# Kernel optimization log

Measured on AMD Instinct MI355X. Metric: run time of the kernel, lower is better.

Reference implementation:

```python
import jax, jax.numpy as jnp
import numpy as np

B, L, LH, D, H = 32, 512, 2048, 1024, 4
DK = D // H  # dot-attn head dim
NEG = -1e9


def _ln(x, g, b, eps=1e-5):
    m = x.mean(-1, keepdims=True)
    v = ((x - m) ** 2).mean(-1, keepdims=True)
    return (x - m) / jnp.sqrt(v + eps) * g + b


def setup_inputs() -> dict:
    key = jax.random.key(0)
    ks = jax.random.split(key, 16)
    s = 0.05
    inp = {
        "seq_emb": jax.random.normal(ks[0], (B, L, D), jnp.float32),
        "seq_mask": jnp.ones((B, L), jnp.float32),
        "his_seq_emb": jax.random.normal(ks[1], (B, LH, D), jnp.float32),
        "his_seq_mask": jnp.ones((B, LH), jnp.float32),
        # dot-product MHA (bias=True)
        "sa_wq": jax.random.normal(ks[2], (D, D), jnp.float32) * s,
        "sa_bq": jnp.zeros((D,), jnp.float32),
        "sa_wk": jax.random.normal(ks[3], (D, D), jnp.float32) * s,
        "sa_bk": jnp.zeros((D,), jnp.float32),
        "sa_wv": jax.random.normal(ks[4], (D, D), jnp.float32) * s,
        "sa_bv": jnp.zeros((D,), jnp.float32),
        "sa_wo": jax.random.normal(ks[5], (D, D), jnp.float32) * s,
        "sa_bo": jnp.zeros((D,), jnp.float32),
        # short LayerNorm
        "sn_g": jnp.ones((D,), jnp.float32),
        "sn_b": jnp.zeros((D,), jnp.float32),
        # additive MHA (h=1, bias=False)
        "aa_wq": jax.random.normal(ks[6], (D, D), jnp.float32) * s,
        "aa_wk": jax.random.normal(ks[7], (D, D), jnp.float32) * s,
        "aa_wv": jax.random.normal(ks[8], (D, D), jnp.float32) * s,
        "aa_wo": jax.random.normal(ks[9], (D, D), jnp.float32) * s,
        "aa_wa": jax.random.normal(ks[10], (D,), jnp.float32) * s,
        # long LayerNorm
        "ln_g": jnp.ones((D,), jnp.float32),
        "ln_b": jnp.zeros((D,), jnp.float32),
    }
    return inp


def reference(seq_emb, seq_mask, his_seq_emb, his_seq_mask,
              sa_wq, sa_bq, sa_wk, sa_bk, sa_wv, sa_bv, sa_wo, sa_bo,
              sn_g, sn_b, aa_wq, aa_wk, aa_wv, aa_wo, aa_wa, ln_g, ln_b):
    # ---- dot-product self attention over seq_emb (dropout = eval/no-op) ----
    def split_heads(x):  # (B,L,D) -> (B,H,L,DK)
        return x.reshape(B, -1, H, DK).transpose(0, 2, 1, 3)

    q = split_heads(seq_emb @ sa_wq + sa_bq)
    k = split_heads(seq_emb @ sa_wk + sa_bk)
    v = split_heads(seq_emb @ sa_wv + sa_bv)
    scores = jnp.einsum('bhqd,bhkd->bhqk', q, k) / jnp.sqrt(jnp.float32(DK))
    scores = jnp.where(seq_mask[:, None, None, :] == 0, NEG, scores)
    p_attn = jax.nn.softmax(scores, axis=-1)  # (B,H,L,L)
    ctx = jnp.einsum('bhqk,bhkd->bhqd', p_attn, v)
    ctx = ctx.transpose(0, 2, 1, 3).reshape(B, L, D)
    sa_out = ctx @ sa_wo + sa_bo

    poi_attn = _ln(sa_out, sn_g, sn_b) * seq_mask[:, :, None]
    poi_hidden = poi_attn.mean(axis=1, keepdims=True)  # (B,1,D)

    # ---- additive (Bahdanau) attention, h=1, Lq=1 ----
    aq = poi_hidden @ aa_wq        # (B,1,D)
    ak = his_seq_emb @ aa_wk       # (B,LH,D)
    av = his_seq_emb @ aa_wv       # (B,LH,D)
    feats = jnp.tanh(aq[:, :, None, :] + ak[:, None, :, :])  # (B,1,LH,D)
    a_scores = jnp.einsum('bqkd,d->bqk', feats, aa_wa)        # (B,1,LH)
    a_scores = jnp.where(his_seq_mask[:, None, :] == 0, NEG, a_scores)
    a_w = jax.nn.softmax(a_scores, axis=-1)
    a_ctx = jnp.einsum('bqk,bkd->bqd', a_w, av)               # (B,1,D)
    aa_out = a_ctx @ aa_wo

    his_poi_hidden = poi_hidden + _ln(aa_out, ln_g, ln_b)     # (B,1,D)

    attn_weight = p_attn[:, 0, :, :]                          # (B,L,L)
    seq_hidden = jnp.concatenate([poi_hidden, his_poi_hidden], axis=-1)[:, 0, :]  # (B,2D)
    return seq_hidden, attn_weight
```

## Files before the change

kernel.cpp:

```cpp
#include <hip/hip_runtime.h>

#define NEGV (-1000000000.0f)

typedef __attribute__((ext_vector_type(8))) short sh8;
typedef __attribute__((ext_vector_type(4))) short sh4;
typedef __attribute__((ext_vector_type(8))) __bf16 bf16x8;
typedef __attribute__((ext_vector_type(4))) float f32x4;

__device__ __forceinline__ float b2f(unsigned short u) {
  unsigned v = ((unsigned)u) << 16;
  return __builtin_bit_cast(float, v);
}
__device__ __forceinline__ unsigned short f2b(float f) {
  unsigned x = __builtin_bit_cast(unsigned, f);
  unsigned r = (x + 0x7fffu + ((x >> 16) & 1u)) >> 16;
  return (unsigned short)r;
}
__device__ __forceinline__ void g2l16(const void* g, void* l) {
  __builtin_amdgcn_global_load_lds((const __attribute__((address_space(1))) unsigned int*)g,
                                   (__attribute__((address_space(3))) unsigned int*)l, 16, 0, 0);
}
__device__ __forceinline__ f32x4 mfma16(bf16x8 a, bf16x8 b, f32x4 c) {
  return __builtin_amdgcn_mfma_f32_16x16x32_bf16(a, b, c, 0, 0, 0);
}
__device__ __forceinline__ float fast_tanh(float x) {
  x = fminf(fmaxf(x, -15.f), 15.f);
  float e = __expf(2.f * x);
  return (e - 1.f) / (e + 1.f);
}

__global__ void cvt_all(const float* __restrict__ sa, unsigned short* __restrict__ da, int n4a,
                        const float* __restrict__ sb, unsigned short* __restrict__ db, int n4b)
{
  int stride = gridDim.x * blockDim.x;
  int i0 = blockIdx.x * blockDim.x + threadIdx.x;
  for (int i = i0; i < n4a; i += stride) {
    float4 v = ((const float4*)sa)[i];
    sh4 o;
    o[0] = (short)f2b(v.x); o[1] = (short)f2b(v.y);
    o[2] = (short)f2b(v.z); o[3] = (short)f2b(v.w);
    ((sh4*)da)[i] = o;
  }
  for (int i = i0; i < n4b; i += stride) {
    float4 v = ((const float4*)sb)[i];
    sh4 o;
    o[0] = (short)f2b(v.x); o[1] = (short)f2b(v.y);
    o[2] = (short)f2b(v.z); o[3] = (short)f2b(v.w);
    ((sh4*)db)[i] = o;
  }
}

__global__ void tcvt5(const float* __restrict__ s0, const float* __restrict__ s1,
                      const float* __restrict__ s2, const float* __restrict__ s3,
                      const float* __restrict__ s4,
                      unsigned short* __restrict__ d0, unsigned short* __restrict__ d1,
                      unsigned short* __restrict__ d2, unsigned short* __restrict__ d3,
                      unsigned short* __restrict__ d4)
{
  __shared__ float tile[64][65];
  const float* src; unsigned short* dst;
  switch (blockIdx.z) {
    case 0: src = s0; dst = d0; break;
    case 1: src = s1; dst = d1; break;
    case 2: src = s2; dst = d2; break;
    case 3: src = s3; dst = d3; break;
    default: src = s4; dst = d4; break;
  }
  int bx = blockIdx.x, by = blockIdx.y;
  int tx = threadIdx.x & 63, ty = threadIdx.x >> 6;
#pragma unroll
  for (int i = 0; i < 16; ++i) {
    int r = i * 4 + ty;
    tile[r][tx] = src[(size_t)(by * 64 + r) * 1024 + bx * 64 + tx];
  }
  __syncthreads();
#pragma unroll
  for (int i = 0; i < 16; ++i) {
    int r = i * 4 + ty;
    dst[(size_t)(bx * 64 + r) * 1024 + by * 64 + tx] = f2b(tile[tx][r]);
  }
}

template<int EPI>
__global__ __launch_bounds__(256, 4)
void gemm128(const unsigned short* __restrict__ A, const unsigned short* __restrict__ Bt,
             int nbx,
             const float* __restrict__ b0, const float* __restrict__ b1,
             const float* __restrict__ b2,
             unsigned short* __restrict__ O0, unsigned short* __restrict__ O1,
             unsigned short* __restrict__ O2,
             const float* __restrict__ aq, const float* __restrict__ wa,
             float* __restrict__ sc)
{
  __shared__ unsigned short ldsA[4096];
  __shared__ unsigned short ldsB[4096];
  const int tid = threadIdx.x;
  const int w = tid >> 6, l = tid & 63;
  const int wr = w >> 1, wc = w & 1;
  const int lr = l & 15, g = l >> 4;

  const int wg = blockIdx.x;
  const int cpx = gridDim.x >> 3;
  const int wgid = (wg & 7) * cpx + (wg >> 3);
  const int bx = wgid % nbx, by = wgid / nbx;
  const size_t m0 = (size_t)by * 128;
  const int n0 = bx * 128;

  f32x4 acc[4][4] = {};

  const int srow = tid >> 2;
  const int sk = ((tid & 3) ^ ((tid >> 2) & 3)) * 8;
  const unsigned short* gA = A + (m0 + srow) * 1024 + sk;
  const unsigned short* gB = Bt + ((size_t)n0 + srow) * 1024 + sk;
  char* const dA0 = (char*)ldsA + w * 1024;
  char* const dA1 = (char*)ldsA + 4096 + w * 1024;
  char* const dB0 = (char*)ldsB + w * 1024;
  char* const dB1 = (char*)ldsB + 4096 + w * 1024;

  const int cswz = (g ^ (lr & 3)) * 16;
  const int aoff = (wr * 64 + lr) * 64 + cswz;
  const int boff = (wc * 64 + lr) * 64 + cswz;

#pragma unroll 1
  for (int kt = 0; kt < 32; ++kt) {
    const int k0 = kt * 32;
    g2l16(gA + k0, dA0);
    g2l16(gA + 64 * 1024 + k0, dA1);
    g2l16(gB + k0, dB0);
    g2l16(gB + 64 * 1024 + k0, dB1);
    __syncthreads();
    bf16x8 af[4], bf[4];
#pragma unroll
    for (int i = 0; i < 4; ++i)
      af[i] = *(const bf16x8*)((const char*)ldsA + aoff + i * 1024);
#pragma unroll
    for (int j = 0; j < 4; ++j)
      bf[j] = *(const bf16x8*)((const char*)ldsB + boff + j * 1024);
#pragma unroll
    for (int i = 0; i < 4; ++i)
#pragma unroll
      for (int j = 0; j < 4; ++j)
        acc[i][j] = mfma16(af[i], bf[j], acc[i][j]);
    __syncthreads();
  }

  if (EPI == 0) {
#pragma unroll
    for (int j = 0; j < 4; ++j) {
      int col = n0 + wc * 64 + j * 16 + lr;
      float bv = b0[col];
#pragma unroll
      for (int i = 0; i < 4; ++i) {
        size_t rowb = m0 + wr * 64 + i * 16 + g * 4;
#pragma unroll
        for (int r = 0; r < 4; ++r)
          O0[(rowb + r) * 1024 + col] = f2b(acc[i][j][r] + bv);
      }
    }
  } else if (EPI == 1) {
#pragma unroll
    for (int j = 0; j < 4; ++j) {
      int col3 = n0 + wc * 64 + j * 16 + lr;
      int part = col3 >> 10, c = col3 & 1023;
      float bv = (part == 0) ? b0[c] : (part == 1) ? b1[c] : b2[c];
      if (part < 2) {
        unsigned short* O = part == 0 ? O0 : O1;
#pragma unroll
        for (int i = 0; i < 4; ++i) {
          size_t rowb = m0 + wr * 64 + i * 16 + g * 4;
#pragma unroll
          for (int r = 0; r < 4; ++r)
            O[(rowb + r) * 1024 + c] = f2b(acc[i][j][r] + bv);
        }
      } else {
        int h = c >> 8, d = c & 255;
#pragma unroll
        for (int i = 0; i < 4; ++i) {
          size_t row = m0 + wr * 64 + i * 16 + g * 4;
          int bb = (int)(row >> 9), ll = (int)(row & 511);
          size_t base = ((size_t)(bb * 4 + h) * 256 + d) * 512 + ll;
#pragma unroll
          for (int r = 0; r < 4; ++r)
            O2[base + r] = f2b(acc[i][j][r] + bv);
        }
      }
    }
  } else {
    const int bb = (int)(m0 >> 11);
#pragma unroll
    for (int i = 0; i < 4; ++i) {
      float rp[4] = {0.f, 0.f, 0.f, 0.f};
#pragma unroll
      for (int j = 0; j < 4; ++j) {
        int col = n0 + wc * 64 + j * 16 + lr;
        float wav = wa[col];
        float aqv = aq[bb * 1024 + col];
#pragma unroll
        for (int r = 0; r < 4; ++r)
          rp[r] += wav * fast_tanh(acc[i][j][r] + aqv);
      }
#pragma unroll
      for (int off = 1; off < 16; off <<= 1)
#pragma unroll
        for (int r = 0; r < 4; ++r)
          rp[r] += __shfl_xor(rp[r], off, 64);
      if (lr == 0) {
        size_t rowb = m0 + wr * 64 + i * 16 + g * 4;
#pragma unroll
        for (int r = 0; r < 4; ++r)
          atomicAdd(&sc[rowb + r], rp[r]);
      }
    }
  }
}

__global__ __launch_bounds__(256, 4)
void attn_kernel(const unsigned short* __restrict__ q, const unsigned short* __restrict__ k,
                 const unsigned short* __restrict__ vT, const float* __restrict__ seq_mask,
                 unsigned short* __restrict__ ctx, float* __restrict__ attn_out)
{
  __shared__ char smem[34304];
  unsigned short* Qs = (unsigned short*)smem;
  unsigned short* Ps = (unsigned short*)smem;
  float* redm = (float*)(smem + 33280);
  float* reds = (float*)(smem + 33792);
  const int t = threadIdx.x, w = t >> 6, l = t & 63;
  const int lr = l & 15, g = l >> 4, lk8 = g * 8;
  const int wg = blockIdx.x;
  const int wgid = (wg & 7) * 256 + (wg >> 3);
  const int qt = wgid & 15, bh = wgid >> 4;
  const int h = bh & 3, b = bh >> 2;
  const int l0 = qt * 32;

  for (int idx = t; idx < 32 * 32; idx += 256) {
    int r = idx >> 5, ch = (idx & 31) * 8;
    *(sh8*)&Qs[r * 264 + ch] =
        *(const sh8*)&q[((size_t)(b * 512 + l0 + r)) * 1024 + h * 256 + ch];
  }
  __syncthreads();

  f32x4 accs[2][8] = {};
  const unsigned short* kbase = k + ((size_t)b * 512) * 1024 + h * 256;
#pragma unroll
  for (int ds = 0; ds < 8; ++ds) {
    int d0 = ds * 32;
    bf16x8 a0 = *(const bf16x8*)&Qs[lr * 264 + d0 + lk8];
    bf16x8 a1 = *(const bf16x8*)&Qs[(16 + lr) * 264 + d0 + lk8];
#pragma unroll
    for (int j = 0; j < 8; ++j) {
      int kj = w * 128 + j * 16 + lr;
      bf16x8 bb = *(const bf16x8*)&kbase[(size_t)kj * 1024 + d0 + lk8];
      accs[0][j] = mfma16(a0, bb, accs[0][j]);
      accs[1][j] = mfma16(a1, bb, accs[1][j]);
    }
  }

#pragma unroll
  for (int j = 0; j < 8; ++j) {
    int col = w * 128 + j * 16 + lr;
    float mv = seq_mask[b * 512 + col];
    bool msk = (mv == 0.f);
#pragma unroll
    for (int i = 0; i < 2; ++i)
#pragma unroll
      for (int r = 0; r < 4; ++r)
        accs[i][j][r] = msk ? NEGV : accs[i][j][r] * 0.0625f;
  }

  float mx[2][4], sm[2][4];
#pragma unroll
  for (int i = 0; i < 2; ++i)
#pragma unroll
    for (int r = 0; r < 4; ++r) {
      float m = accs[i][0][r];
#pragma unroll
      for (int j = 1; j < 8; ++j) m = fmaxf(m, accs[i][j][r]);
      mx[i][r] = m;
    }
#pragma unroll
  for (int off = 1; off < 16; off <<= 1)
#pragma unroll
    for (int i = 0; i < 2; ++i)
#pragma unroll
      for (int r = 0; r < 4; ++r)
        mx[i][r] = fmaxf(mx[i][r], __shfl_xor(mx[i][r], off, 64));
  if (lr == 0) {
#pragma unroll
    for (int i = 0; i < 2; ++i)
#pragma unroll
      for (int r = 0; r < 4; ++r)
        redm[w * 32 + i * 16 + g * 4 + r] = mx[i][r];
  }
  __syncthreads();
#pragma unroll
  for (int i = 0; i < 2; ++i)
#pragma unroll
    for (int r = 0; r < 4; ++r) {
      int row = i * 16 + g * 4 + r;
      mx[i][r] = fmaxf(fmaxf(redm[row], redm[32 + row]),
                       fmaxf(redm[64 + row], redm[96 + row]));
      sm[i][r] = 0.f;
    }

#pragma unroll
  for (int i = 0; i < 2; ++i)
#pragma unroll
    for (int j = 0; j < 8; ++j)
#pragma unroll
      for (int r = 0; r < 4; ++r) {
        float p = __expf(accs[i][j][r] - mx[i][r]);
        accs[i][j][r] = p;
        sm[i][r] += p;
      }
#pragma unroll
  for (int off = 1; off < 16; off <<= 1)
#pragma unroll
    for (int i = 0; i < 2; ++i)
#pragma unroll
      for (int r = 0; r < 4; ++r)
        sm[i][r] += __shfl_xor(sm[i][r], off, 64);
  if (lr == 0) {
#pragma unroll
    for (int i = 0; i < 2; ++i)
#pragma unroll
      for (int r = 0; r < 4; ++r)
        reds[w * 32 + i * 16 + g * 4 + r] = sm[i][r];
  }
  __syncthreads();
#pragma unroll
  for (int i = 0; i < 2; ++i)
#pragma unroll
    for (int r = 0; r < 4; ++r) {
      int row = i * 16 + g * 4 + r;
      float s = reds[row] + reds[32 + row] + reds[64 + row] + reds[96 + row];
      sm[i][r] = 1.f / s;
    }

#pragma unroll
  for (int i = 0; i < 2; ++i)
#pragma unroll
    for (int j = 0; j < 8; ++j) {
      int col = w * 128 + j * 16 + lr;
#pragma unroll
      for (int r = 0; r < 4; ++r) {
        int row = i * 16 + g * 4 + r;
        float pn = accs[i][j][r] * sm[i][r];
        Ps[row * 520 + col] = f2b(pn);
        if (h == 0)
          attn_out[((size_t)(b * 512 + l0 + row)) * 512 + col] = pn;
      }
    }
  __syncthreads();

  f32x4 acco[2][4] = {};
  const unsigned short* vbase = vT + ((size_t)(b * 4 + h)) * 256 * 512;
#pragma unroll
  for (int ks = 0; ks < 16; ++ks) {
    int kj0 = ks * 32;
    bf16x8 a0 = *(const bf16x8*)&Ps[lr * 520 + kj0 + lk8];
    bf16x8 a1 = *(const bf16x8*)&Ps[(16 + lr) * 520 + kj0 + lk8];
#pragma unroll
    for (int j = 0; j < 4; ++j) {
      int d = w * 64 + j * 16 + lr;
      bf16x8 bb = *(const bf16x8*)&vbase[(size_t)d * 512 + kj0 + lk8];
      acco[0][j] = mfma16(a0, bb, acco[0][j]);
      acco[1][j] = mfma16(a1, bb, acco[1][j]);
    }
  }
#pragma unroll
  for (int i = 0; i < 2; ++i)
#pragma unroll
    for (int j = 0; j < 4; ++j) {
      int col = w * 64 + j * 16 + lr;
#pragma unroll
      for (int r = 0; r < 4; ++r) {
        int row = i * 16 + g * 4 + r;
        ctx[((size_t)(b * 512 + l0 + row)) * 1024 + h * 256 + col] = f2b(acco[i][j][r]);
      }
    }
}

__global__ __launch_bounds__(256)
void ln_mean(const unsigned short* __restrict__ sa, const float* __restrict__ g,
             const float* __restrict__ bt, const float* __restrict__ mask,
             float* __restrict__ poi_sum)
{
  const int b = blockIdx.y, ch = blockIdx.x;
  const int t = threadIdx.x, w = t >> 6, l = t & 63;
  float gg[16], bb[16];
#pragma unroll
  for (int j = 0; j < 16; ++j) { gg[j] = g[l * 16 + j]; bb[j] = bt[l * 16 + j]; }
  float accv[16];
#pragma unroll
  for (int j = 0; j < 16; ++j) accv[j] = 0.f;
  for (int rr = 0; rr < 16; ++rr) {
    int row = ch * 64 + w * 16 + rr;
    const unsigned short* rp = sa + ((size_t)(b * 512 + row)) * 1024 + l * 16;
    float x[16];
    sh8 v0 = *(const sh8*)rp;
    sh8 v1 = *(const sh8*)(rp + 8);
#pragma unroll
    for (int j = 0; j < 8; ++j) {
      x[j] = b2f((unsigned short)v0[j]);
      x[8 + j] = b2f((unsigned short)v1[j]);
    }
    float s = 0.f, s2 = 0.f;
#pragma unroll
    for (int j = 0; j < 16; ++j) { s += x[j]; s2 += x[j] * x[j]; }
#pragma unroll
    for (int off = 1; off < 64; off <<= 1) {
      s += __shfl_xor(s, off, 64);
      s2 += __shfl_xor(s2, off, 64);
    }
    float mean = s * (1.f / 1024.f);
    float var = s2 * (1.f / 1024.f) - mean * mean;
    float rinv = rsqrtf(var + 1e-5f);
    float mk = mask[b * 512 + row];
#pragma unroll
    for (int j = 0; j < 16; ++j) accv[j] += ((x[j] - mean) * rinv * gg[j] + bb[j]) * mk;
  }
#pragma unroll
  for (int j = 0; j < 16; ++j) atomicAdd(&poi_sum[b * 1024 + l * 16 + j], accv[j]);
}

__global__ __launch_bounds__(256)
void poi_gemv(const float* __restrict__ ps, const float* __restrict__ wq,
              float* __restrict__ poi, float* __restrict__ aq)
{
  const int b = blockIdx.y;
  const int n = blockIdx.x * 256 + threadIdx.x;
  const float* ib = ps + b * 1024;
  float acc = 0.f;
  for (int d = 0; d < 1024; d += 4) {
    acc += ib[d]     * wq[(size_t)d * 1024 + n]
         + ib[d + 1] * wq[(size_t)(d + 1) * 1024 + n]
         + ib[d + 2] * wq[(size_t)(d + 2) * 1024 + n]
         + ib[d + 3] * wq[(size_t)(d + 3) * 1024 + n];
  }
  poi[b * 1024 + n] = ib[n] * (1.f / 512.f);
  aq[b * 1024 + n] = acc * (1.f / 512.f);
}

__global__ __launch_bounds__(256)
void gemv32(const float* __restrict__ in, const float* __restrict__ W, float* __restrict__ out)
{
  const int b = blockIdx.y;
  const int n = blockIdx.x * 256 + threadIdx.x;
  const float* ib = in + b * 1024;
  float acc = 0.f;
  for (int d = 0; d < 1024; d += 4) {
    acc += ib[d]     * W[(size_t)d * 1024 + n]
         + ib[d + 1] * W[(size_t)(d + 1) * 1024 + n]
         + ib[d + 2] * W[(size_t)(d + 2) * 1024 + n]
         + ib[d + 3] * W[(size_t)(d + 3) * 1024 + n];
  }
  out[b * 1024 + n] = acc;
}

__global__ __launch_bounds__(256)
void softmax_his(float* __restrict__ sc, const float* __restrict__ mask)
{
  __shared__ float red[4];
  const int b = blockIdx.x, t = threadIdx.x, w = t >> 6, l = t & 63;
  float v[8];
  float mx = -3.0e38f;
#pragma unroll
  for (int i = 0; i < 8; ++i) {
    int kk = t + i * 256;
    float s = (mask[b * 2048 + kk] == 0.f) ? NEGV : sc[b * 2048 + kk];
    v[i] = s;
    mx = fmaxf(mx, s);
  }
#pragma unroll
  for (int off = 1; off < 64; off <<= 1) mx = fmaxf(mx, __shfl_xor(mx, off, 64));
  if (l == 0) red[w] = mx;
  __syncthreads();
  mx = fmaxf(fmaxf(red[0], red[1]), fmaxf(red[2], red[3]));
  float sum = 0.f;
#pragma unroll
  for (int i = 0; i < 8; ++i) { v[i] = __expf(v[i] - mx); sum += v[i]; }
#pragma unroll
  for (int off = 1; off < 64; off <<= 1) sum += __shfl_xor(sum, off, 64);
  __syncthreads();
  if (l == 0) red[w] = sum;
  __syncthreads();
  sum = red[0] + red[1] + red[2] + red[3];
  float inv = 1.f / sum;
#pragma unroll
  for (int i = 0; i < 8; ++i) sc[b * 2048 + t + i * 256] = v[i] * inv;
}

__global__ __launch_bounds__(256)
void hw_kernel(const float* __restrict__ aw, const unsigned short* __restrict__ his,
               float* __restrict__ hw)
{
  const int b = blockIdx.y, kc = blockIdx.x, t = threadIdx.x;
  const int cb = t * 4;
  float a0 = 0.f, a1 = 0.f, a2 = 0.f, a3 = 0.f;
  for (int kk = 0; kk < 256; ++kk) {
    int k = kc * 256 + kk;
    float wg = aw[b * 2048 + k];
    sh4 vv = *(const sh4*)&his[((size_t)(b * 2048 + k)) * 1024 + cb];
    a0 += wg * b2f((unsigned short)vv[0]);
    a1 += wg * b2f((unsigned short)vv[1]);
    a2 += wg * b2f((unsigned short)vv[2]);
    a3 += wg * b2f((unsigned short)vv[3]);
  }
  atomicAdd(&hw[b * 1024 + cb + 0], a0);
  atomicAdd(&hw[b * 1024 + cb + 1], a1);
  atomicAdd(&hw[b * 1024 + cb + 2], a2);
  atomicAdd(&hw[b * 1024 + cb + 3], a3);
}

__global__ __launch_bounds__(256)
void final_kernel(const float* __restrict__ aa_out, const float* __restrict__ g,
                  const float* __restrict__ bt, const float* __restrict__ poi,
                  float* __restrict__ out)
{
  __shared__ float r1[4], r2[4];
  const int b = blockIdx.x, t = threadIdx.x, w = t >> 6, l = t & 63;
  float x[4];
#pragma unroll
  for (int j = 0; j < 4; ++j) x[j] = aa_out[b * 1024 + t * 4 + j];
  float s = 0.f, s2 = 0.f;
#pragma unroll
  for (int j = 0; j < 4; ++j) { s += x[j]; s2 += x[j] * x[j]; }
#pragma unroll
  for (int off = 1; off < 64; off <<= 1) {
    s += __shfl_xor(s, off, 64);
    s2 += __shfl_xor(s2, off, 64);
  }
  if (l == 0) { r1[w] = s; r2[w] = s2; }
  __syncthreads();
  s = r1[0] + r1[1] + r1[2] + r1[3];
  s2 = r2[0] + r2[1] + r2[2] + r2[3];
  float mean = s * (1.f / 1024.f);
  float var = s2 * (1.f / 1024.f) - mean * mean;
  float rinv = rsqrtf(var + 1e-5f);
#pragma unroll
  for (int j = 0; j < 4; ++j) {
    int c = t * 4 + j;
    float lnv = (x[j] - mean) * rinv * g[c] + bt[c];
    float pv = poi[b * 1024 + c];
    out[b * 2048 + c] = pv;
    out[b * 2048 + 1024 + c] = pv + lnv;
  }
}

extern "C" void kernel_launch(void* const* d_in, const int* in_sizes, int n_in,
                              void* d_out, int out_size, void* d_ws, size_t ws_size,
                              hipStream_t stream)
{
  const float* seq_emb  = (const float*)d_in[0];
  const float* seq_mask = (const float*)d_in[1];
  const float* his_emb  = (const float*)d_in[2];
  const float* his_mask = (const float*)d_in[3];
  const float* sa_wq = (const float*)d_in[4];
  const float* sa_bq = (const float*)d_in[5];
  const float* sa_wk = (const float*)d_in[6];
  const float* sa_bk = (const float*)d_in[7];
  const float* sa_wv = (const float*)d_in[8];
  const float* sa_bv = (const float*)d_in[9];
  const float* sa_wo = (const float*)d_in[10];
  const float* sa_bo = (const float*)d_in[11];
  const float* sn_g  = (const float*)d_in[12];
  const float* sn_b  = (const float*)d_in[13];
  const float* aa_wq = (const float*)d_in[14];
  const float* aa_wk = (const float*)d_in[15];
  const float* aa_wv = (const float*)d_in[16];
  const float* aa_wo = (const float*)d_in[17];
  const float* aa_wa = (const float*)d_in[18];
  const float* ln_g  = (const float*)d_in[19];
  const float* ln_b  = (const float*)d_in[20];
  float* out = (float*)d_out;

  char* p = (char*)d_ws;
  size_t off = 0;
  auto alloc = [&](size_t bytes) -> void* {
    void* r = p + off;
    off += (bytes + 255) & ~(size_t)255;
    return r;
  };
  unsigned short* seqb = (unsigned short*)alloc((size_t)16384 * 1024 * 2);
  unsigned short* hisb = (unsigned short*)alloc((size_t)65536 * 1024 * 2);
  unsigned short* wcat = (unsigned short*)alloc((size_t)3072 * 1024 * 2);
  unsigned short* woT  = (unsigned short*)alloc((size_t)1024 * 1024 * 2);
  unsigned short* awkT = (unsigned short*)alloc((size_t)1024 * 1024 * 2);
  unsigned short* qb   = (unsigned short*)alloc((size_t)16384 * 1024 * 2);
  unsigned short* kb   = (unsigned short*)alloc((size_t)16384 * 1024 * 2);
  unsigned short* vTb  = (unsigned short*)alloc((size_t)16384 * 1024 * 2);
  unsigned short* ctxb = (unsigned short*)alloc((size_t)16384 * 1024 * 2);
  unsigned short* saob = (unsigned short*)alloc((size_t)16384 * 1024 * 2);
  float* poi_sum = (float*)alloc((size_t)32 * 1024 * 4);
  float* poi     = (float*)alloc((size_t)32 * 1024 * 4);
  float* aqb     = (float*)alloc((size_t)32 * 1024 * 4);
  float* ascore  = (float*)alloc((size_t)32 * 2048 * 4);
  float* hwb     = (float*)alloc((size_t)32 * 1024 * 4);
  float* actx    = (float*)alloc((size_t)32 * 1024 * 4);
  float* aaout   = (float*)alloc((size_t)32 * 1024 * 4);
  if (off > ws_size) return;

  hipMemsetAsync(poi_sum, 0, (size_t)32 * 1024 * 4, stream);
  hipMemsetAsync(ascore, 0, (size_t)32 * 2048 * 4, stream);
  hipMemsetAsync(hwb, 0, (size_t)32 * 1024 * 4, stream);

  cvt_all<<<2048, 256, 0, stream>>>(seq_emb, seqb, 16384 * 1024 / 4,
                                    his_emb, hisb, 65536 * 1024 / 4);
  tcvt5<<<dim3(16, 16, 5), 256, 0, stream>>>(
      sa_wq, sa_wk, sa_wv, sa_wo, aa_wk,
      wcat, wcat + (size_t)1024 * 1024, wcat + (size_t)2048 * 1024, woT, awkT);

  gemm128<1><<<3072, 256, 0, stream>>>(seqb, wcat, 24, sa_bq, sa_bk, sa_bv,
                                       qb, kb, vTb, nullptr, nullptr, nullptr);

  attn_kernel<<<2048, 256, 0, stream>>>(qb, kb, vTb, seq_mask, ctxb, out + 65536);

  gemm128<0><<<1024, 256, 0, stream>>>(ctxb, woT, 8, sa_bo, nullptr, nullptr,
                                       saob, nullptr, nullptr, nullptr, nullptr, nullptr);
  ln_mean<<<dim3(8, 32), 256, 0, stream>>>(saob, sn_g, sn_b, seq_mask, poi_sum);
  poi_gemv<<<dim3(4, 32), 256, 0, stream>>>(poi_sum, aa_wq, poi, aqb);

  gemm128<2><<<4096, 256, 0, stream>>>(hisb, awkT, 8, nullptr, nullptr, nullptr,
                                       nullptr, nullptr, nullptr, aqb, aa_wa, ascore);
  softmax_his<<<32, 256, 0, stream>>>(ascore, his_mask);
  hw_kernel<<<dim3(8, 32), 256, 0, stream>>>(ascore, hisb, hwb);
  gemv32<<<dim3(4, 32), 256, 0, stream>>>(hwb, aa_wv, actx);
  gemv32<<<dim3(4, 32), 256, 0, stream>>>(actx, aa_wo, aaout);
  final_kernel<<<32, 256, 0, stream>>>(aaout, ln_g, ln_b, poi, out);
}
```

Measured before the change: 815.2 us.

## Fuse prep, softmax+weighted-sum, and tail gemvs; change LDS swizzle; merge memsets

Merges the two conversion kernels into one prep launch, fuses the history softmax into the weighted-sum kernel (each block recomputes the softmax redundantly), and folds the two gemvs and the final layernorm into one 32-block tail kernel. It also changes the XOR swizzle used for LDS staging in the GEMM and replaces three memsets with one contiguous memset. Fewer launches cut overhead, but the tail kernel runs only 32 blocks that each stream two full 1024x1024 fp32 weight matrices, which may serialize poorly on the GPU.

```diff
diff --git a/kernel.cpp b/kernel.cpp
--- a/kernel.cpp
+++ b/kernel.cpp
@@ -29,45 +29,48 @@
   return (e - 1.f) / (e + 1.f);
 }
 
-__global__ void cvt_all(const float* __restrict__ sa, unsigned short* __restrict__ da, int n4a,
-                        const float* __restrict__ sb, unsigned short* __restrict__ db, int n4b)
-{
-  int stride = gridDim.x * blockDim.x;
-  int i0 = blockIdx.x * blockDim.x + threadIdx.x;
-  for (int i = i0; i < n4a; i += stride) {
-    float4 v = ((const float4*)sa)[i];
-    sh4 o;
-    o[0] = (short)f2b(v.x); o[1] = (short)f2b(v.y);
-    o[2] = (short)f2b(v.z); o[3] = (short)f2b(v.w);
-    ((sh4*)da)[i] = o;
-  }
-  for (int i = i0; i < n4b; i += stride) {
-    float4 v = ((const float4*)sb)[i];
-    sh4 o;
-    o[0] = (short)f2b(v.x); o[1] = (short)f2b(v.y);
-    o[2] = (short)f2b(v.z); o[3] = (short)f2b(v.w);
-    ((sh4*)db)[i] = o;
-  }
-}
-
-__global__ void tcvt5(const float* __restrict__ s0, const float* __restrict__ s1,
-                      const float* __restrict__ s2, const float* __restrict__ s3,
-                      const float* __restrict__ s4,
-                      unsigned short* __restrict__ d0, unsigned short* __restrict__ d1,
-                      unsigned short* __restrict__ d2, unsigned short* __restrict__ d3,
-                      unsigned short* __restrict__ d4)
-{
+__global__ __launch_bounds__(256)
+void prep(const float* __restrict__ seq, unsigned short* __restrict__ seqb, int n4a,
+          const float* __restrict__ his, unsigned short* __restrict__ hisb, int n4b,
+          const float* __restrict__ s0, const float* __restrict__ s1,
+          const float* __restrict__ s2, const float* __restrict__ s3,
+          const float* __restrict__ s4,
+          unsigned short* __restrict__ d0, unsigned short* __restrict__ d1,
+          unsigned short* __restrict__ d2, unsigned short* __restrict__ d3,
+          unsigned short* __restrict__ d4)
+{
+  const int t = threadIdx.x;
+  if (blockIdx.x < 2048) {
+    const int stride = 2048 * 256;
+    for (int i = blockIdx.x * 256 + t; i < n4a; i += stride) {
+      float4 v = ((const float4*)seq)[i];
+      sh4 o;
+      o[0] = (short)f2b(v.x); o[1] = (short)f2b(v.y);
+      o[2] = (short)f2b(v.z); o[3] = (short)f2b(v.w);
+      ((sh4*)seqb)[i] = o;
+    }
+    for (int i = blockIdx.x * 256 + t; i < n4b; i += stride) {
+      float4 v = ((const float4*)his)[i];
+      sh4 o;
+      o[0] = (short)f2b(v.x); o[1] = (short)f2b(v.y);
+      o[2] = (short)f2b(v.z); o[3] = (short)f2b(v.w);
+      ((sh4*)hisb)[i] = o;
+    }
+    return;
+  }
   __shared__ float tile[64][65];
+  int z2 = blockIdx.x - 2048;
+  int zz = z2 >> 8, rem = z2 & 255;
+  int by = rem >> 4, bx = rem & 15;
   const float* src; unsigned short* dst;
-  switch (blockIdx.z) {
+  switch (zz) {
     case 0: src = s0; dst = d0; break;
     case 1: src = s1; dst = d1; break;
     case 2: src = s2; dst = d2; break;
     case 3: src = s3; dst = d3; break;
     default: src = s4; dst = d4; break;
   }
-  int bx = blockIdx.x, by = blockIdx.y;
-  int tx = threadIdx.x & 63, ty = threadIdx.x >> 6;
+  int tx = t & 63, ty = t >> 6;
 #pragma unroll
   for (int i = 0; i < 16; ++i) {
     int r = i * 4 + ty;
@@ -109,7 +112,7 @@
   f32x4 acc[4][4] = {};
 
   const int srow = tid >> 2;
-  const int sk = ((tid & 3) ^ ((tid >> 2) & 3)) * 8;
+  const int sk = ((tid & 3) ^ ((tid >> 3) & 3)) * 8;
   const unsigned short* gA = A + (m0 + srow) * 1024 + sk;
   const unsigned short* gB = Bt + ((size_t)n0 + srow) * 1024 + sk;
   char* const dA0 = (char*)ldsA + w * 1024;
@@ -117,7 +120,7 @@
   char* const dB0 = (char*)ldsB + w * 1024;
   char* const dB1 = (char*)ldsB + 4096 + w * 1024;
 
-  const int cswz = (g ^ (lr & 3)) * 16;
+  const int cswz = (g ^ ((lr >> 1) & 3)) * 16;
   const int aoff = (wr * 64 + lr) * 64 + cswz;
   const int boff = (wc * 64 + lr) * 64 + cswz;
 
@@ -442,26 +445,13 @@
 }
 
 __global__ __launch_bounds__(256)
-void gemv32(const float* __restrict__ in, const float* __restrict__ W, float* __restrict__ out)
-{
-  const int b = blockIdx.y;
-  const int n = blockIdx.x * 256 + threadIdx.x;
-  const float* ib = in + b * 1024;
-  float acc = 0.f;
-  for (int d = 0; d < 1024; d += 4) {
-    acc += ib[d]     * W[(size_t)d * 1024 + n]
-         + ib[d + 1] * W[(size_t)(d + 1) * 1024 + n]
-         + ib[d + 2] * W[(size_t)(d + 2) * 1024 + n]
-         + ib[d + 3] * W[(size_t)(d + 3) * 1024 + n];
-  }
-  out[b * 1024 + n] = acc;
-}
-
-__global__ __launch_bounds__(256)
-void softmax_his(float* __restrict__ sc, const float* __restrict__ mask)
-{
+void softhw(const float* __restrict__ sc, const float* __restrict__ mask,
+            const unsigned short* __restrict__ his, float* __restrict__ hw)
+{
+  __shared__ float wloc[2048];
   __shared__ float red[4];
-  const int b = blockIdx.x, t = threadIdx.x, w = t >> 6, l = t & 63;
+  const int b = blockIdx.y, kc = blockIdx.x;
+  const int t = threadIdx.x, w = t >> 6, l = t & 63;
   float v[8];
   float mx = -3.0e38f;
 #pragma unroll
@@ -478,28 +468,24 @@
   mx = fmaxf(fmaxf(red[0], red[1]), fmaxf(red[2], red[3]));
   float sum = 0.f;
 #pragma unroll
-  for (int i = 0; i < 8; ++i) { v[i] = __expf(v[i] - mx); sum += v[i]; }
+  for (int i = 0; i < 8; ++i) {
+    v[i] = __expf(v[i] - mx);
+    wloc[t + i * 256] = v[i];
+    sum += v[i];
+  }
 #pragma unroll
   for (int off = 1; off < 64; off <<= 1) sum += __shfl_xor(sum, off, 64);
   __syncthreads();
   if (l == 0) red[w] = sum;
   __syncthreads();
   sum = red[0] + red[1] + red[2] + red[3];
-  float inv = 1.f / sum;
-#pragma unroll
-  for (int i = 0; i < 8; ++i) sc[b * 2048 + t + i * 256] = v[i] * inv;
-}
-
-__global__ __launch_bounds__(256)
-void hw_kernel(const float* __restrict__ aw, const unsigned short* __restrict__ his,
-               float* __restrict__ hw)
-{
-  const int b = blockIdx.y, kc = blockIdx.x, t = threadIdx.x;
+  const float inv = 1.f / sum;
+
   const int cb = t * 4;
   float a0 = 0.f, a1 = 0.f, a2 = 0.f, a3 = 0.f;
   for (int kk = 0; kk < 256; ++kk) {
     int k = kc * 256 + kk;
-    float wg = aw[b * 2048 + k];
+    float wg = wloc[k] * inv;
     sh4 vv = *(const sh4*)&his[((size_t)(b * 2048 + k)) * 1024 + cb];
     a0 += wg * b2f((unsigned short)vv[0]);
     a1 += wg * b2f((unsigned short)vv[1]);
@@ -513,15 +499,42 @@
 }
 
 __global__ __launch_bounds__(256)
-void final_kernel(const float* __restrict__ aa_out, const float* __restrict__ g,
-                  const float* __restrict__ bt, const float* __restrict__ poi,
-                  float* __restrict__ out)
-{
+void tail(const float* __restrict__ hwb, const float* __restrict__ wv,
+          const float* __restrict__ wo, const float* __restrict__ g,
+          const float* __restrict__ bt, const float* __restrict__ poi,
+          float* __restrict__ out)
+{
+  __shared__ float hl[1024];
+  __shared__ float al[1024];
   __shared__ float r1[4], r2[4];
   const int b = blockIdx.x, t = threadIdx.x, w = t >> 6, l = t & 63;
-  float x[4];
-#pragma unroll
-  for (int j = 0; j < 4; ++j) x[j] = aa_out[b * 1024 + t * 4 + j];
+
+  for (int i = t; i < 1024; i += 256) hl[i] = hwb[b * 1024 + i];
+  __syncthreads();
+
+  float a[4] = {0.f, 0.f, 0.f, 0.f};
+  for (int d = 0; d < 1024; ++d) {
+    float hv = hl[d];
+    const float* wr = wv + (size_t)d * 1024 + t;
+    a[0] += hv * wr[0];
+    a[1] += hv * wr[256];
+    a[2] += hv * wr[512];
+    a[3] += hv * wr[768];
+  }
+#pragma unroll
+  for (int j = 0; j < 4; ++j) al[t + j * 256] = a[j];
+  __syncthreads();
+
+  float x[4] = {0.f, 0.f, 0.f, 0.f};
+  for (int d = 0; d < 1024; ++d) {
+    float xv = al[d];
+    const float* wr = wo + (size_t)d * 1024 + t;
+    x[0] += xv * wr[0];
+    x[1] += xv * wr[256];
+    x[2] += xv * wr[512];
+    x[3] += xv * wr[768];
+  }
+
   float s = 0.f, s2 = 0.f;
 #pragma unroll
   for (int j = 0; j < 4; ++j) { s += x[j]; s2 += x[j] * x[j]; }
@@ -539,7 +552,7 @@
   float rinv = rsqrtf(var + 1e-5f);
 #pragma unroll
   for (int j = 0; j < 4; ++j) {
-    int c = t * 4 + j;
+    int c = t + j * 256;
     float lnv = (x[j] - mean) * rinv * g[c] + bt[c];
     float pv = poi[b * 1024 + c];
     out[b * 2048 + c] = pv;
@@ -596,19 +609,15 @@
   float* aqb     = (float*)alloc((size_t)32 * 1024 * 4);
   float* ascore  = (float*)alloc((size_t)32 * 2048 * 4);
   float* hwb     = (float*)alloc((size_t)32 * 1024 * 4);
-  float* actx    = (float*)alloc((size_t)32 * 1024 * 4);
-  float* aaout   = (float*)alloc((size_t)32 * 1024 * 4);
   if (off > ws_size) return;
 
-  hipMemsetAsync(poi_sum, 0, (size_t)32 * 1024 * 4, stream);
-  hipMemsetAsync(ascore, 0, (size_t)32 * 2048 * 4, stream);
-  hipMemsetAsync(hwb, 0, (size_t)32 * 1024 * 4, stream);
-
-  cvt_all<<<2048, 256, 0, stream>>>(seq_emb, seqb, 16384 * 1024 / 4,
-                                    his_emb, hisb, 65536 * 1024 / 4);
-  tcvt5<<<dim3(16, 16, 5), 256, 0, stream>>>(
-      sa_wq, sa_wk, sa_wv, sa_wo, aa_wk,
-      wcat, wcat + (size_t)1024 * 1024, wcat + (size_t)2048 * 1024, woT, awkT);
+  hipMemsetAsync(poi_sum, 0, (size_t)(6 * 32 * 1024) * 4, stream);
+
+  prep<<<3328, 256, 0, stream>>>(seq_emb, seqb, 16384 * 1024 / 4,
+                                 his_emb, hisb, 65536 * 1024 / 4,
+                                 sa_wq, sa_wk, sa_wv, sa_wo, aa_wk,
+                                 wcat, wcat + (size_t)1024 * 1024,
+                                 wcat + (size_t)2048 * 1024, woT, awkT);
 
   gemm128<1><<<3072, 256, 0, stream>>>(seqb, wcat, 24, sa_bq, sa_bk, sa_bv,
                                        qb, kb, vTb, nullptr, nullptr, nullptr);
@@ -622,9 +631,6 @@
 
   gemm128<2><<<4096, 256, 0, stream>>>(hisb, awkT, 8, nullptr, nullptr, nullptr,
                                        nullptr, nullptr, nullptr, aqb, aa_wa, ascore);
-  softmax_his<<<32, 256, 0, stream>>>(ascore, his_mask);
-  hw_kernel<<<dim3(8, 32), 256, 0, stream>>>(ascore, hisb, hwb);
-  gemv32<<<dim3(4, 32), 256, 0, stream>>>(hwb, aa_wv, actx);
-  gemv32<<<dim3(4, 32), 256, 0, stream>>>(actx, aa_wo, aaout);
-  final_kernel<<<32, 256, 0, stream>>>(aaout, ln_g, ln_b, poi, out);
-}
+  softhw<<<dim3(8, 32), 256, 0, stream>>>(ascore, his_mask, hisb, hwb);
+  tail<<<32, 256, 0, stream>>>(hwb, aa_wv, aa_wo, ln_g, ln_b, poi, out);
+}
```

Result: slower. 896.8 us (+10.0%).
